# Optimization experiments

Measured on AMD Instinct MI355X. Metric: run time of the kernel, lower is better.

## Reference

```python
import jax, jax.numpy as jnp
import numpy as np

N = 50000      # nodes
E = 1600000    # edges (avg degree 32)
G = 128        # graphs in batch
NE = 5         # spectral supports (edge_attr channels)
NIN = 16       # input node features
H = 64         # nout1 hidden width
NCLS = 6
BN_EPS = 1e-5


def setup_inputs() -> dict:
    key = jax.random.key(0)
    ks = jax.random.split(key, 12)
    s = 0.1  # weight init scale
    x = jax.random.normal(ks[0], (N, NIN), dtype=jnp.float32)
    edge_index = jax.random.randint(ks[1], (2, E), 0, N, dtype=jnp.int32)
    edge_attr = jax.random.normal(ks[2], (E, NE), dtype=jnp.float32)
    # sorted segment ids covering all G graphs (non-empty segments)
    batch = ((jnp.arange(N, dtype=jnp.int32) * G) // N).astype(jnp.int32)
    W1 = jax.random.normal(ks[3], (NE, NIN, H), dtype=jnp.float32) * s
    W2 = jax.random.normal(ks[4], (NE, H, H), dtype=jnp.float32) * s
    W3 = jax.random.normal(ks[5], (NE, H, H), dtype=jnp.float32) * s
    W4 = jax.random.normal(ks[6], (NE, H, H), dtype=jnp.float32) * s
    b1 = jnp.zeros((H,), jnp.float32)
    b2 = jnp.zeros((H,), jnp.float32)
    b3 = jnp.zeros((H,), jnp.float32)
    b4 = jnp.zeros((H,), jnp.float32)
    bn_gamma = jnp.ones((2 * H,), jnp.float32)
    bn_beta = jnp.zeros((2 * H,), jnp.float32)
    bn_mean = jax.random.normal(ks[7], (2 * H,), dtype=jnp.float32)
    bn_var = jax.random.uniform(ks[8], (2 * H,), dtype=jnp.float32) + 0.5
    fc_w = jax.random.normal(ks[9], (2 * H, NCLS), dtype=jnp.float32) * s
    fc_b = jnp.zeros((NCLS,), jnp.float32)
    return {"x": x, "edge_index": edge_index, "edge_attr": edge_attr,
            "batch": batch, "W1": W1, "b1": b1, "W2": W2, "b2": b2,
            "W3": W3, "b3": b3, "W4": W4, "b4": b4,
            "bn_gamma": bn_gamma, "bn_beta": bn_beta,
            "bn_mean": bn_mean, "bn_var": bn_var,
            "fc_w": fc_w, "fc_b": fc_b}


def spect_conv(x, src, dst, edge_attr, W, b):
    # SpectConv(selfconn=False): out = sum_k scatter_add(edge_attr[:,k]*x[src] -> dst) @ W[k] + b
    xs = x[src]  # [E, F] gather
    n = x.shape[0]
    out = jnp.zeros((n, W.shape[2]), x.dtype)
    for k in range(W.shape[0]):  # K=5 spectral supports
        h = jax.ops.segment_sum(edge_attr[:, k:k + 1] * xs, dst, num_segments=n)
        out = out + h @ W[k]
    return out + b


def reference(x, edge_index, edge_attr, batch, W1, b1, W2, b2, W3, b3, W4, b4,
              bn_gamma, bn_beta, bn_mean, bn_var, fc_w, fc_b):
    src, dst = edge_index[0], edge_index[1]
    h = jax.nn.relu(spect_conv(x, src, dst, edge_attr, W1, b1))
    h = jax.nn.relu(spect_conv(h, src, dst, edge_attr, W2, b2))
    h = jax.nn.relu(spect_conv(h, src, dst, edge_attr, W3, b3))
    h = jax.nn.relu(spect_conv(h, src, dst, edge_attr, W4, b4))
    pooled = jnp.concatenate([
        jax.ops.segment_sum(h, batch, num_segments=G),
        jax.ops.segment_max(h, batch, num_segments=G)], axis=1)  # [G, 2H]
    bn = (pooled - bn_mean) * jax.lax.rsqrt(bn_var + BN_EPS) * bn_gamma + bn_beta
    return jax.nn.log_softmax(bn @ fc_w + fc_b, axis=1)
```

## Files before the change

### kernel.cpp

```cpp
#include <hip/hip_runtime.h>


#define Nn   50000
#define Ne   1600000
#define Gg   128
#define NEk  5
#define NINf 16
#define NCLSo 6
#define NB   196
#define RBK  128
#define CHK  (Ne / RBK)

using short8 = __attribute__((ext_vector_type(8))) short;
using f32x4  = __attribute__((ext_vector_type(4))) float;
using f32x2  = __attribute__((ext_vector_type(2))) float;
using uint4v = __attribute__((ext_vector_type(4))) unsigned;

__device__ __forceinline__ float2 bf2u(unsigned u) {
    return make_float2(__uint_as_float(u << 16), __uint_as_float(u & 0xffff0000u));
}
__device__ __forceinline__ unsigned f2bf(float a, float b) {
    unsigned ua = __float_as_uint(a), ub = __float_as_uint(b);
    ua += 0x7fffu + ((ua >> 16) & 1u);
    ub += 0x7fffu + ((ub >> 16) & 1u);
    return (ua >> 16) | (ub & 0xffff0000u);
}
__device__ __forceinline__ unsigned short f2bf1(float a) {
    unsigned ua = __float_as_uint(a);
    ua += 0x7fffu + ((ua >> 16) & 1u);
    return (unsigned short)(ua >> 16);
}

__device__ __forceinline__ f32x2 fma2s(float a, f32x2 x, f32x2 c) {
#if __has_builtin(__builtin_elementwise_fma)
    f32x2 av; av.x = a; av.y = a;
    return __builtin_elementwise_fma(av, x, c);
#else
    c.x = fmaf(a, x.x, c.x); c.y = fmaf(a, x.y, c.y);
    return c;
#endif
}


__global__ void k_pad_x(const float* __restrict__ x, unsigned* __restrict__ h0) {
    int i = blockIdx.x * 256 + threadIdx.x;
    if (i >= Nn * 32) return;
    int n = i >> 5, p = i & 31;
    int f0 = 2 * p;
    float v0 = (f0 < NINf) ? x[n * NINf + f0] : 0.f;
    float v1 = (f0 + 1 < NINf) ? x[n * NINf + f0 + 1] : 0.f;
    h0[i] = f2bf(v0, v1);
}

__global__ void k_pad_w1(const float* __restrict__ W1, float* __restrict__ W1p) {
    int i = blockIdx.x * 256 + threadIdx.x;
    if (i >= NEk * 64 * 64) return;
    int h = i & 63, f = (i >> 6) & 63, k = i >> 12;
    W1p[i] = (f < NINf) ? W1[(k * NINf + f) * 64 + h] : 0.f;
}

__global__ void k_pack_b(const float* __restrict__ W, unsigned short* __restrict__ bhi,
                         unsigned short* __restrict__ blo) {
    int i = blockIdx.x * 256 + threadIdx.x;
    if (i >= 20480) return;
    int j = i & 7, lane = (i >> 3) & 63, t2 = i >> 9;
    int nt = t2 / 10, kstep = t2 - nt * 10;
    int k = kstep * 32 + (lane >> 4) * 8 + j;
    int col = nt * 16 + (lane & 15);
    float v = W[k * 64 + col];
    unsigned short hi = f2bf1(v);
    float fhi = __uint_as_float(((unsigned)hi) << 16);
    bhi[i] = hi;
    blo[i] = f2bf1(v - fhi);
}

__global__ __launch_bounds__(1024) void k_rankhist(
    const int* __restrict__ ei, unsigned short* __restrict__ lrank,
    unsigned short* __restrict__ cnt ) {
    __shared__ unsigned hist[12500];
    int b = blockIdx.x, t = threadIdx.x;
    int e0 = b * CHK;
    for (int w = t; w < 12500; w += 1024) hist[w] = 0;
    __syncthreads();
    for (int i = t; i < CHK; i += 1024) {
        int d = ei[Ne + e0 + i];
        unsigned sh = 8u * (unsigned)(d & 3);
        unsigned old = atomicAdd(&hist[d >> 2], 1u << sh);
        lrank[e0 + i] = (unsigned short)((old >> sh) & 0xffu);
    }
    __syncthreads();
    unsigned* co = (unsigned*)(cnt + (size_t)b * Nn);
    for (int w = t; w < 12500; w += 1024) {
        unsigned hv = hist[w];
        co[2 * w]     = (hv & 0xffu) | ((hv >> 8) & 0xffu) << 16;
        co[2 * w + 1] = ((hv >> 16) & 0xffu) | (hv >> 24) << 16;
    }
}

__global__ void k_colscan(unsigned short* __restrict__ cnt, int* __restrict__ deg) {
    int d = blockIdx.x * 256 + threadIdx.x;
    if (d >= Nn) return;
    int s = 0;
#pragma unroll 4
    for (int b = 0; b < RBK; ++b) {
        int t = cnt[(size_t)b * Nn + d];
        cnt[(size_t)b * Nn + d] = (unsigned short)s;
        s += t;
    }
    deg[d] = s;
}


__global__ void k_blocksum(const int* __restrict__ deg, int* __restrict__ bsum) {
    __shared__ int l[256];
    int t = threadIdx.x;
    int i = blockIdx.x * 256 + t;
    l[t] = (i < Nn) ? deg[i] : 0;
    __syncthreads();
    for (int off = 128; off > 0; off >>= 1) {
        if (t < off) l[t] += l[t + off];
        __syncthreads();
    }
    if (t == 0) bsum[blockIdx.x] = l[0];
}

__global__ void k_scanpart(const int* __restrict__ bsum, int* __restrict__ boff) {
    __shared__ int l[256];
    int t = threadIdx.x;
    int v = (t < NB) ? bsum[t] : 0;
    l[t] = v;
    __syncthreads();
    for (int off = 1; off < 256; off <<= 1) {
        int u = (t >= off) ? l[t - off] : 0;
        __syncthreads();
        l[t] += u;
        __syncthreads();
    }
    if (t < NB) boff[t] = l[t] - v;
}

__global__ void k_scanfinal(const int* __restrict__ deg, const int* __restrict__ boff,
                            int* __restrict__ rowstart) {
    __shared__ int l[256];
    int t = threadIdx.x;
    int i = blockIdx.x * 256 + t;
    int v = (i < Nn) ? deg[i] : 0;
    l[t] = v;
    __syncthreads();
    for (int off = 1; off < 256; off <<= 1) {
        int u = (t >= off) ? l[t - off] : 0;
        __syncthreads();
        l[t] += u;
        __syncthreads();
    }
    if (i <= Nn) rowstart[i] = boff[blockIdx.x] + l[t] - v;
}

__global__ __launch_bounds__(256) void k_place(
    const int* __restrict__ ei, const float* __restrict__ eattr,
    const int* __restrict__ rowstart,
    const unsigned short* __restrict__ lrank,
    const unsigned short* __restrict__ cnt,
    unsigned* __restrict__ recs ) {
    int e = (blockIdx.x * 256 + threadIdx.x) * 4;
    if (e >= Ne) return;
    int b = e / CHK;
    const unsigned short* cb = cnt + (size_t)b * Nn;

    int4 dv = *(const int4*)(ei + Ne + e);
    int4 sv = *(const int4*)(ei + e);
    ushort4 lr = *(const ushort4*)(lrank + e);
    union { float4 v4[5]; float f[20]; } a;
#pragma unroll
    for (int q = 0; q < 5; ++q) a.v4[q] = *(const float4*)(eattr + (size_t)e * 5 + q * 4);

    int d[4] = { dv.x, dv.y, dv.z, dv.w };
    int s[4] = { sv.x, sv.y, sv.z, sv.w };
    unsigned short r4[4] = { lr.x, lr.y, lr.z, lr.w };
    int pos[4];
#pragma unroll
    for (int j = 0; j < 4; ++j)
        pos[j] = rowstart[d[j]] + cb[d[j]] + r4[j];
#pragma unroll
    for (int j = 0; j < 4; ++j) {
        uint4v rr;
        rr.x = (unsigned)s[j];
        rr.y = f2bf(a.f[5 * j],     a.f[5 * j + 1]);
        rr.z = f2bf(a.f[5 * j + 2], a.f[5 * j + 3]);
        rr.w = f2bf(a.f[5 * j + 4], 0.f);
        __builtin_nontemporal_store(rr, (uint4v*)(recs + (size_t)pos[j] * 4));
    }
}

__global__ void k_bounds(const int* __restrict__ batch, int* __restrict__ sg,
                         int* __restrict__ eg) {
    int n = blockIdx.x * 256 + threadIdx.x;
    if (n >= Nn) return;
    int g = batch[n];
    if (n == 0) sg[g] = 0;
    else {
        int gp = batch[n - 1];
        if (gp != g) { sg[g] = n; eg[gp] = n; }
    }
    if (n == Nn - 1) eg[g] = Nn;
}


__global__ __launch_bounds__(256) void k_aggregate(
    const unsigned* __restrict__ hin, const int* __restrict__ rowstart,
    const uint4* __restrict__ recs, unsigned* __restrict__ agg) {
    int lane = threadIdx.x & 63;
    int l = lane & 31, half = lane >> 5;
    int node = __builtin_amdgcn_readfirstlane((int)(blockIdx.x * 4 + (threadIdx.x >> 6)));
    int beg = rowstart[node], end = rowstart[node + 1];
    f32x2 c0 = {0.f, 0.f}, c1 = c0, c2 = c0, c3 = c0, c4 = c0;
    int ee = beg;
#define EDGE(E) { \
    uint4 r = recs[(E)]; \
    unsigned hx = hin[(size_t)(int)r.x * 32 + l]; \
    f32x2 xv; xv.x = __uint_as_float(hx << 16); xv.y = __uint_as_float(hx & 0xffff0000u); \
    float A0 = __uint_as_float(r.y << 16), A1 = __uint_as_float(r.y & 0xffff0000u); \
    float A2 = __uint_as_float(r.z << 16), A3 = __uint_as_float(r.z & 0xffff0000u); \
    float A4 = __uint_as_float(r.w << 16); \
    c0 = fma2s(A0, xv, c0); c1 = fma2s(A1, xv, c1); \
    c2 = fma2s(A2, xv, c2); c3 = fma2s(A3, xv, c3); \
    c4 = fma2s(A4, xv, c4); }
    for (; ee + 8 <= end; ee += 8) {
        EDGE(ee + half) EDGE(ee + 2 + half) EDGE(ee + 4 + half) EDGE(ee + 6 + half)
    }
    for (; ee + 2 <= end; ee += 2) { EDGE(ee + half) }
    if (ee < end) { if (half == 0) { EDGE(ee) } }
#undef EDGE
    c0.x += __shfl(c0.x, lane ^ 32); c0.y += __shfl(c0.y, lane ^ 32);
    c1.x += __shfl(c1.x, lane ^ 32); c1.y += __shfl(c1.y, lane ^ 32);
    c2.x += __shfl(c2.x, lane ^ 32); c2.y += __shfl(c2.y, lane ^ 32);
    c3.x += __shfl(c3.x, lane ^ 32); c3.y += __shfl(c3.y, lane ^ 32);
    c4.x += __shfl(c4.x, lane ^ 32); c4.y += __shfl(c4.y, lane ^ 32);
    if (half == 0) {
        unsigned* o = agg + (size_t)node * 160 + l;
        o[0]   = f2bf(c0.x, c0.y);
        o[32]  = f2bf(c1.x, c1.y);
        o[64]  = f2bf(c2.x, c2.y);
        o[96]  = f2bf(c3.x, c3.y);
        o[128] = f2bf(c4.x, c4.y);
    }
}

#define SPAD 41
__global__ __launch_bounds__(256) void k_transform(
    const uint4* __restrict__ A, const unsigned short* __restrict__ bhi,
    const unsigned short* __restrict__ blo, const float* __restrict__ bias,
    unsigned* __restrict__ outh) {
    __shared__ uint4 smem[64 * SPAD];
    int t = threadIdx.x;
    int lane = t & 63, wave = t >> 6;
    int m = lane & 15, quad = lane >> 4;
    int blk = blockIdx.x;

#pragma unroll
    for (int it = 0; it < 10; ++it) {
        int v = t + it * 256;
        int row = v / 40, off = v - row * 40;
        int node = blk * 64 + row;
        if (node >= Nn) node = Nn - 1;
        smem[row * SPAD + off] = A[(size_t)node * 40 + off];
    }
    __syncthreads();

    f32x4 acc0 = {0.f, 0.f, 0.f, 0.f}, acc1 = acc0, acc2 = acc0, acc3 = acc0;
    const uint4* arow = smem + (wave * 16 + m) * SPAD + quad;
#pragma unroll 2
    for (int ks = 0; ks < 10; ++ks) {
        short8 a = *(const short8*)(arow + ks * 4);
        size_t bb = ((size_t)ks * 64 + lane) * 8;
        short8 h0 = *(const short8*)(bhi + bb);
        short8 l0 = *(const short8*)(blo + bb);
        acc0 = __builtin_amdgcn_mfma_f32_16x16x32_bf16(a, h0, acc0, 0, 0, 0);
        acc0 = __builtin_amdgcn_mfma_f32_16x16x32_bf16(a, l0, acc0, 0, 0, 0);
        short8 h1 = *(const short8*)(bhi + bb + 5120);
        short8 l1 = *(const short8*)(blo + bb + 5120);
        acc1 = __builtin_amdgcn_mfma_f32_16x16x32_bf16(a, h1, acc1, 0, 0, 0);
        acc1 = __builtin_amdgcn_mfma_f32_16x16x32_bf16(a, l1, acc1, 0, 0, 0);
        short8 h2 = *(const short8*)(bhi + bb + 10240);
        short8 l2 = *(const short8*)(blo + bb + 10240);
        acc2 = __builtin_amdgcn_mfma_f32_16x16x32_bf16(a, h2, acc2, 0, 0, 0);
        acc2 = __builtin_amdgcn_mfma_f32_16x16x32_bf16(a, l2, acc2, 0, 0, 0);
        short8 h3 = *(const short8*)(bhi + bb + 15360);
        short8 l3 = *(const short8*)(blo + bb + 15360);
        acc3 = __builtin_amdgcn_mfma_f32_16x16x32_bf16(a, h3, acc3, 0, 0, 0);
        acc3 = __builtin_amdgcn_mfma_f32_16x16x32_bf16(a, l3, acc3, 0, 0, 0);
    }
    __syncthreads();

    float* Cs = (float*)smem;
#pragma unroll
    for (int r = 0; r < 4; ++r) {
        int base = wave * 1152 + (quad * 4 + r) * 72 + m;
        Cs[base]      = acc0[r];
        Cs[base + 16] = acc1[r];
        Cs[base + 32] = acc2[r];
        Cs[base + 48] = acc3[r];
    }
    __syncthreads();

    int row = t >> 2, grp = t & 3;
    int node = blk * 64 + row;
    if (node < Nn) {
        const float* cr = Cs + (row >> 4) * 1152 + (row & 15) * 72;
        unsigned o[8];
#pragma unroll
        for (int j = 0; j < 8; ++j) {
            int pp = grp * 8 + j;
            float v0 = fmaxf(cr[2 * pp]     + bias[2 * pp],     0.f);
            float v1 = fmaxf(cr[2 * pp + 1] + bias[2 * pp + 1], 0.f);
            o[j] = f2bf(v0, v1);
        }
        uint4* dst = (uint4*)(outh + (size_t)node * 32 + grp * 8);
        dst[0] = make_uint4(o[0], o[1], o[2], o[3]);
        dst[1] = make_uint4(o[4], o[5], o[6], o[7]);
    }
}


__global__ __launch_bounds__(256) void k_pool(const unsigned* __restrict__ h,
                                              const int* __restrict__ sg,
                                              const int* __restrict__ eg,
                                              float* __restrict__ pooled) {
    __shared__ float2 ls[256], lm[256];
    int g = blockIdx.x, t = threadIdx.x;
    int p = t & 31, q = t >> 5;
    int s = sg[g], e = eg[g];
    float2 sum = {0.f, 0.f}, mx = {0.f, 0.f};
    for (int n = s + q; n < e; n += 8) {
        float2 v = bf2u(h[(size_t)n * 32 + p]);
        sum.x += v.x; sum.y += v.y;
        mx.x = fmaxf(mx.x, v.x); mx.y = fmaxf(mx.y, v.y);
    }
    ls[t] = sum; lm[t] = mx;
    __syncthreads();
    if (t < 32) {
        float2 ss = ls[t], mm = lm[t];
        for (int i = 1; i < 8; ++i) {
            float2 a = ls[t + i * 32], b = lm[t + i * 32];
            ss.x += a.x; ss.y += a.y;
            mm.x = fmaxf(mm.x, b.x); mm.y = fmaxf(mm.y, b.y);
        }
        pooled[g * 128 + 2 * t]          = ss.x;
        pooled[g * 128 + 2 * t + 1]      = ss.y;
        pooled[g * 128 + 64 + 2 * t]     = mm.x;
        pooled[g * 128 + 64 + 2 * t + 1] = mm.y;
    }
}

__global__ void k_head(const float* __restrict__ pooled, const float* __restrict__ gamma,
                       const float* __restrict__ beta, const float* __restrict__ mean,
                       const float* __restrict__ var, const float* __restrict__ fcw,
                       const float* __restrict__ fcb, float* __restrict__ out) {
    __shared__ float y[128];
    __shared__ float lg[8];
    int g = blockIdx.x, c = threadIdx.x;
    float p = pooled[g * 128 + c];
    y[c] = (p - mean[c]) * rsqrtf(var[c] + 1e-5f) * gamma[c] + beta[c];
    __syncthreads();
    if (c < NCLSo) {
        float l = fcb[c];
        for (int i = 0; i < 128; ++i) l += y[i] * fcw[i * NCLSo + c];
        lg[c] = l;
    }
    __syncthreads();
    if (c == 0) {
        float m = lg[0];
        for (int j = 1; j < NCLSo; ++j) m = fmaxf(m, lg[j]);
        float se = 0.f;
        for (int j = 0; j < NCLSo; ++j) se += expf(lg[j] - m);
        float lse = m + logf(se);
        for (int j = 0; j < NCLSo; ++j) out[g * NCLSo + j] = lg[j] - lse;
    }
}


static inline size_t rup(size_t x) { return (x + 255) & ~(size_t)255; }

extern "C" void kernel_launch(void* const* d_in, const int* in_sizes, int n_in,
                              void* d_out, int out_size, void* d_ws, size_t ws_size,
                              hipStream_t stream) {
    const float* x     = (const float*)d_in[0];
    const int*   ei    = (const int*)d_in[1];
    const float* eattr = (const float*)d_in[2];
    const int*   batch = (const int*)d_in[3];
    const float* W1    = (const float*)d_in[4];
    const float* b1    = (const float*)d_in[5];
    const float* W2    = (const float*)d_in[6];
    const float* b2    = (const float*)d_in[7];
    const float* W3    = (const float*)d_in[8];
    const float* b3    = (const float*)d_in[9];
    const float* W4    = (const float*)d_in[10];
    const float* b4    = (const float*)d_in[11];
    const float* gamma = (const float*)d_in[12];
    const float* beta  = (const float*)d_in[13];
    const float* mean  = (const float*)d_in[14];
    const float* var   = (const float*)d_in[15];
    const float* fcw   = (const float*)d_in[16];
    const float* fcb   = (const float*)d_in[17];
    float* out = (float*)d_out;

    char* p = (char*)d_ws;
    auto take = [&](size_t bytes) { char* r = p; p += rup(bytes); return r; };
    int*            deg      = (int*)take((size_t)(Nn + 1) * 4);
    unsigned short* cnt      = (unsigned short*)take((size_t)RBK * Nn * 2);
    unsigned short* lrank    = (unsigned short*)take((size_t)Ne * 2);
    int*            rowstart = (int*)take((size_t)(Nn + 1) * 4);
    int*            bsum     = (int*)take((size_t)NB * 4);
    int*            boff     = (int*)take((size_t)NB * 4);
    uint4*          recs     = (uint4*)take((size_t)Ne * 16);
    unsigned*       hA       = (unsigned*)take((size_t)Nn * 32 * 4);
    unsigned*       hB       = (unsigned*)take((size_t)Nn * 32 * 4);
    unsigned*       agg      = (unsigned*)take((size_t)Nn * 160 * 4);
    float*          W1p      = (float*)take((size_t)NEk * 64 * 64 * 4);
    unsigned short* bhiA     = (unsigned short*)take((size_t)4 * 20480 * 2);
    unsigned short* bloA     = (unsigned short*)take((size_t)4 * 20480 * 2);
    float*          pooled   = (float*)take((size_t)Gg * 128 * 4);
    int*            sg       = (int*)take((size_t)Gg * 4);
    int*            eg       = (int*)take((size_t)Gg * 4);

    k_rankhist<<<RBK, 1024, 0, stream>>>(ei, lrank, cnt);
    k_pad_x<<<(Nn * 32 + 255) / 256, 256, 0, stream>>>(x, hA);
    k_pad_w1<<<(NEk * 64 * 64 + 255) / 256, 256, 0, stream>>>(W1, W1p);
    k_pack_b<<<80, 256, 0, stream>>>(W1p, bhiA,             bloA);
    k_pack_b<<<80, 256, 0, stream>>>(W2,  bhiA + 20480,     bloA + 20480);
    k_pack_b<<<80, 256, 0, stream>>>(W3,  bhiA + 2 * 20480, bloA + 2 * 20480);
    k_pack_b<<<80, 256, 0, stream>>>(W4,  bhiA + 3 * 20480, bloA + 3 * 20480);
    k_colscan<<<NB, 256, 0, stream>>>(cnt, deg);
    k_blocksum<<<NB, 256, 0, stream>>>(deg, bsum);
    k_scanpart<<<1, 256, 0, stream>>>(bsum, boff);
    k_scanfinal<<<NB, 256, 0, stream>>>(deg, boff, rowstart);
    k_place<<<(Ne / 4 + 255) / 256, 256, 0, stream>>>(ei, eattr, rowstart, lrank, cnt,
                                                      (unsigned*)recs);
    k_bounds<<<(Nn + 255) / 256, 256, 0, stream>>>(batch, sg, eg);

    const float* bs[4] = { b1, b2, b3, b4 };
    unsigned* cur = hA;
    unsigned* nxt = hB;
    for (int L = 0; L < 4; ++L) {
        k_aggregate<<<Nn / 4, 256, 0, stream>>>(cur, rowstart, recs, agg);
        k_transform<<<(Nn + 63) / 64, 256, 0, stream>>>(
            (const uint4*)agg, bhiA + (size_t)L * 20480, bloA + (size_t)L * 20480,
            bs[L], nxt);
        unsigned* tmp = cur; cur = nxt; nxt = tmp;
    }

    k_pool<<<Gg, 256, 0, stream>>>(cur, sg, eg, pooled);
    k_head<<<Gg, 128, 0, stream>>>(pooled, gamma, beta, mean, var, fcw, fcb, out);
}
```

Measured before the change: 500.6 us.

## Fuse edge aggregation and MFMA transform into one per-layer kernel

Merges the per-layer aggregate and transform kernels into one kernel. Each block handles 32 nodes, with each wave aggregating 8 nodes serially into shared memory. The block then runs the MFMA weight transform directly from LDS, with waves split by output column tile. This removes the bf16 aggregate buffer round trip through global memory (160 words per node) and one launch per layer. In exchange, each wave processes nodes sequentially, which reduces memory-level parallelism in the gather-heavy aggregation and may lengthen the critical path per block.

```diff
diff --git a/kernel.cpp b/kernel.cpp
--- a/kernel.cpp
+++ b/kernel.cpp
@@ -205,16 +205,28 @@
     if (n == Nn - 1) eg[g] = Nn;
 }
 
-
-__global__ __launch_bounds__(256) void k_aggregate(
+#define SPAD 41
+__global__ __launch_bounds__(256) void k_layer32(
     const unsigned* __restrict__ hin, const int* __restrict__ rowstart,
-    const uint4* __restrict__ recs, unsigned* __restrict__ agg) {
-    int lane = threadIdx.x & 63;
+    const uint4* __restrict__ recs, const unsigned short* __restrict__ bhi,
+    const unsigned short* __restrict__ blo, const float* __restrict__ bias,
+    unsigned* __restrict__ outh) {
+    __shared__ uint4 smem[32 * SPAD];
+    unsigned* aggw = (unsigned*)smem;
+    int t = threadIdx.x;
+    int lane = t & 63, wave = t >> 6;
     int l = lane & 31, half = lane >> 5;
-    int node = __builtin_amdgcn_readfirstlane((int)(blockIdx.x * 4 + (threadIdx.x >> 6)));
-    int beg = rowstart[node], end = rowstart[node + 1];
-    f32x2 c0 = {0.f, 0.f}, c1 = c0, c2 = c0, c3 = c0, c4 = c0;
-    int ee = beg;
+    int blk = blockIdx.x;
+
+#pragma unroll 1
+    for (int ni = 0; ni < 8; ++ni) {
+        int row = wave * 8 + ni;
+        int node = blk * 32 + row;
+        if (node >= Nn) node = Nn - 1;
+        node = __builtin_amdgcn_readfirstlane(node);
+        int beg = rowstart[node], end = rowstart[node + 1];
+        f32x2 c0 = {0.f, 0.f}, c1 = c0, c2 = c0, c3 = c0, c4 = c0;
+        int ee = beg;
 #define EDGE(E) { \
     uint4 r = recs[(E)]; \
     unsigned hx = hin[(size_t)(int)r.x * 32 + l]; \
@@ -225,99 +237,72 @@
     c0 = fma2s(A0, xv, c0); c1 = fma2s(A1, xv, c1); \
     c2 = fma2s(A2, xv, c2); c3 = fma2s(A3, xv, c3); \
     c4 = fma2s(A4, xv, c4); }
-    for (; ee + 8 <= end; ee += 8) {
-        EDGE(ee + half) EDGE(ee + 2 + half) EDGE(ee + 4 + half) EDGE(ee + 6 + half)
-    }
-    for (; ee + 2 <= end; ee += 2) { EDGE(ee + half) }
-    if (ee < end) { if (half == 0) { EDGE(ee) } }
+        for (; ee + 8 <= end; ee += 8) {
+            EDGE(ee + half) EDGE(ee + 2 + half) EDGE(ee + 4 + half) EDGE(ee + 6 + half)
+        }
+        for (; ee + 2 <= end; ee += 2) { EDGE(ee + half) }
+        if (ee < end) { if (half == 0) { EDGE(ee) } }
 #undef EDGE
-    c0.x += __shfl(c0.x, lane ^ 32); c0.y += __shfl(c0.y, lane ^ 32);
-    c1.x += __shfl(c1.x, lane ^ 32); c1.y += __shfl(c1.y, lane ^ 32);
-    c2.x += __shfl(c2.x, lane ^ 32); c2.y += __shfl(c2.y, lane ^ 32);
-    c3.x += __shfl(c3.x, lane ^ 32); c3.y += __shfl(c3.y, lane ^ 32);
-    c4.x += __shfl(c4.x, lane ^ 32); c4.y += __shfl(c4.y, lane ^ 32);
-    if (half == 0) {
-        unsigned* o = agg + (size_t)node * 160 + l;
-        o[0]   = f2bf(c0.x, c0.y);
-        o[32]  = f2bf(c1.x, c1.y);
-        o[64]  = f2bf(c2.x, c2.y);
-        o[96]  = f2bf(c3.x, c3.y);
-        o[128] = f2bf(c4.x, c4.y);
-    }
-}
-
-#define SPAD 41
-__global__ __launch_bounds__(256) void k_transform(
-    const uint4* __restrict__ A, const unsigned short* __restrict__ bhi,
-    const unsigned short* __restrict__ blo, const float* __restrict__ bias,
-    unsigned* __restrict__ outh) {
-    __shared__ uint4 smem[64 * SPAD];
-    int t = threadIdx.x;
-    int lane = t & 63, wave = t >> 6;
+        c0.x += __shfl(c0.x, lane ^ 32); c0.y += __shfl(c0.y, lane ^ 32);
+        c1.x += __shfl(c1.x, lane ^ 32); c1.y += __shfl(c1.y, lane ^ 32);
+        c2.x += __shfl(c2.x, lane ^ 32); c2.y += __shfl(c2.y, lane ^ 32);
+        c3.x += __shfl(c3.x, lane ^ 32); c3.y += __shfl(c3.y, lane ^ 32);
+        c4.x += __shfl(c4.x, lane ^ 32); c4.y += __shfl(c4.y, lane ^ 32);
+        if (half == 0) {
+            unsigned* o = aggw + row * (SPAD * 4) + l;
+            o[0]   = f2bf(c0.x, c0.y);
+            o[32]  = f2bf(c1.x, c1.y);
+            o[64]  = f2bf(c2.x, c2.y);
+            o[96]  = f2bf(c3.x, c3.y);
+            o[128] = f2bf(c4.x, c4.y);
+        }
+    }
+    __syncthreads();
+
     int m = lane & 15, quad = lane >> 4;
-    int blk = blockIdx.x;
-
-#pragma unroll
-    for (int it = 0; it < 10; ++it) {
-        int v = t + it * 256;
-        int row = v / 40, off = v - row * 40;
-        int node = blk * 64 + row;
-        if (node >= Nn) node = Nn - 1;
-        smem[row * SPAD + off] = A[(size_t)node * 40 + off];
-    }
-    __syncthreads();
-
-    f32x4 acc0 = {0.f, 0.f, 0.f, 0.f}, acc1 = acc0, acc2 = acc0, acc3 = acc0;
-    const uint4* arow = smem + (wave * 16 + m) * SPAD + quad;
+    f32x4 acc0 = {0.f, 0.f, 0.f, 0.f}, acc1 = acc0;
+    const uint4* ar0 = smem + m * SPAD + quad;
+    const uint4* ar1 = smem + (16 + m) * SPAD + quad;
+    const size_t bbase = (size_t)wave * 5120;
 #pragma unroll 2
     for (int ks = 0; ks < 10; ++ks) {
-        short8 a = *(const short8*)(arow + ks * 4);
-        size_t bb = ((size_t)ks * 64 + lane) * 8;
-        short8 h0 = *(const short8*)(bhi + bb);
-        short8 l0 = *(const short8*)(blo + bb);
-        acc0 = __builtin_amdgcn_mfma_f32_16x16x32_bf16(a, h0, acc0, 0, 0, 0);
-        acc0 = __builtin_amdgcn_mfma_f32_16x16x32_bf16(a, l0, acc0, 0, 0, 0);
-        short8 h1 = *(const short8*)(bhi + bb + 5120);
-        short8 l1 = *(const short8*)(blo + bb + 5120);
-        acc1 = __builtin_amdgcn_mfma_f32_16x16x32_bf16(a, h1, acc1, 0, 0, 0);
-        acc1 = __builtin_amdgcn_mfma_f32_16x16x32_bf16(a, l1, acc1, 0, 0, 0);
-        short8 h2 = *(const short8*)(bhi + bb + 10240);
-        short8 l2 = *(const short8*)(blo + bb + 10240);
-        acc2 = __builtin_amdgcn_mfma_f32_16x16x32_bf16(a, h2, acc2, 0, 0, 0);
-        acc2 = __builtin_amdgcn_mfma_f32_16x16x32_bf16(a, l2, acc2, 0, 0, 0);
-        short8 h3 = *(const short8*)(bhi + bb + 15360);
-        short8 l3 = *(const short8*)(blo + bb + 15360);
-        acc3 = __builtin_amdgcn_mfma_f32_16x16x32_bf16(a, h3, acc3, 0, 0, 0);
-        acc3 = __builtin_amdgcn_mfma_f32_16x16x32_bf16(a, l3, acc3, 0, 0, 0);
+        short8 a0 = *(const short8*)(ar0 + ks * 4);
+        short8 a1 = *(const short8*)(ar1 + ks * 4);
+        size_t bb = bbase + ((size_t)ks * 64 + lane) * 8;
+        short8 h = *(const short8*)(bhi + bb);
+        short8 lo = *(const short8*)(blo + bb);
+        acc0 = __builtin_amdgcn_mfma_f32_16x16x32_bf16(a0, h,  acc0, 0, 0, 0);
+        acc0 = __builtin_amdgcn_mfma_f32_16x16x32_bf16(a0, lo, acc0, 0, 0, 0);
+        acc1 = __builtin_amdgcn_mfma_f32_16x16x32_bf16(a1, h,  acc1, 0, 0, 0);
+        acc1 = __builtin_amdgcn_mfma_f32_16x16x32_bf16(a1, lo, acc1, 0, 0, 0);
     }
     __syncthreads();
 
     float* Cs = (float*)smem;
 #pragma unroll
     for (int r = 0; r < 4; ++r) {
-        int base = wave * 1152 + (quad * 4 + r) * 72 + m;
-        Cs[base]      = acc0[r];
-        Cs[base + 16] = acc1[r];
-        Cs[base + 32] = acc2[r];
-        Cs[base + 48] = acc3[r];
-    }
-    __syncthreads();
-
-    int row = t >> 2, grp = t & 3;
-    int node = blk * 64 + row;
-    if (node < Nn) {
-        const float* cr = Cs + (row >> 4) * 1152 + (row & 15) * 72;
-        unsigned o[8];
+        int base = (quad * 4 + r) * 72 + wave * 16 + m;
+        Cs[base]            = acc0[r];
+        Cs[base + 16 * 72]  = acc1[r];
+    }
+    __syncthreads();
+
+    {
+        int row = t >> 3, grp = t & 7;
+        int node = blk * 32 + row;
+        if (node < Nn) {
+            const float* cr = Cs + row * 72;
+            unsigned o[4];
 #pragma unroll
-        for (int j = 0; j < 8; ++j) {
-            int pp = grp * 8 + j;
-            float v0 = fmaxf(cr[2 * pp]     + bias[2 * pp],     0.f);
-            float v1 = fmaxf(cr[2 * pp + 1] + bias[2 * pp + 1], 0.f);
-            o[j] = f2bf(v0, v1);
+            for (int j = 0; j < 4; ++j) {
+                int pp = grp * 4 + j;
+                float v0 = fmaxf(cr[2 * pp]     + bias[2 * pp],     0.f);
+                float v1 = fmaxf(cr[2 * pp + 1] + bias[2 * pp + 1], 0.f);
+                o[j] = f2bf(v0, v1);
+            }
+            *(uint4*)(outh + (size_t)node * 32 + grp * 4) =
+                make_uint4(o[0], o[1], o[2], o[3]);
         }
-        uint4* dst = (uint4*)(outh + (size_t)node * 32 + grp * 8);
-        dst[0] = make_uint4(o[0], o[1], o[2], o[3]);
-        dst[1] = make_uint4(o[4], o[5], o[6], o[7]);
     }
 }
 
@@ -415,7 +400,6 @@
     uint4*          recs     = (uint4*)take((size_t)Ne * 16);
     unsigned*       hA       = (unsigned*)take((size_t)Nn * 32 * 4);
     unsigned*       hB       = (unsigned*)take((size_t)Nn * 32 * 4);
-    unsigned*       agg      = (unsigned*)take((size_t)Nn * 160 * 4);
     float*          W1p      = (float*)take((size_t)NEk * 64 * 64 * 4);
     unsigned short* bhiA     = (unsigned short*)take((size_t)4 * 20480 * 2);
     unsigned short* bloA     = (unsigned short*)take((size_t)4 * 20480 * 2);
@@ -442,9 +426,8 @@
     unsigned* cur = hA;
     unsigned* nxt = hB;
     for (int L = 0; L < 4; ++L) {
-        k_aggregate<<<Nn / 4, 256, 0, stream>>>(cur, rowstart, recs, agg);
-        k_transform<<<(Nn + 63) / 64, 256, 0, stream>>>(
-            (const uint4*)agg, bhiA + (size_t)L * 20480, bloA + (size_t)L * 20480,
+        k_layer32<<<(Nn + 31) / 32, 256, 0, stream>>>(
+            cur, rowstart, recs, bhiA + (size_t)L * 20480, bloA + (size_t)L * 20480,
             bs[L], nxt);
         unsigned* tmp = cur; cur = nxt; nxt = tmp;
     }
```

Result: slower. 554.0 us (+10.7%).
